# Performance work log

Measured on AMD Instinct MI355X. Metric: run time of the kernel, lower is better.

Reference implementation:

```python
import jax, jax.numpy as jnp
import numpy as np

COMMITMENT_COST = 0.25
NUM_EMBEDDINGS = 512
EMBEDDING_DIM = 64


def setup_inputs() -> dict:
    key = jax.random.key(0)
    k1, k2 = jax.random.split(key)
    inputs = jax.random.normal(k1, (32, EMBEDDING_DIM, 64, 64), dtype=jnp.float32)  # B,C,H,W
    embedding = jax.random.normal(k2, (NUM_EMBEDDINGS, EMBEDDING_DIM), dtype=jnp.float32)  # K,D
    return {"inputs": inputs, "embedding": embedding}


def reference(inputs, embedding):
    # Eval-mode forward of VectorQuantizerEMA (training-branch EMA updates are
    # in-place buffer updates, skipped when self.training is False).
    x = jnp.transpose(inputs, (0, 2, 3, 1))            # B,H,W,C
    B, H, W, D = x.shape
    K = embedding.shape[0]
    flat = x.reshape(-1, D)                            # N,D
    d = (jnp.sum(flat * flat, axis=1, keepdims=True)
         + jnp.sum(embedding * embedding, axis=1)
         - 2.0 * flat @ embedding.T)
    indices = jnp.argmin(d, axis=1)                    # N (int)
    # gather == one-hot @ embedding, but without materializing N x K one-hot
    quantized = embedding[indices].reshape(B, H, W, D)
    # commitment loss (quantized is detached in the torch code)
    e_latent_loss = jnp.mean((jax.lax.stop_gradient(quantized) - x) ** 2)
    loss = COMMITMENT_COST * e_latent_loss
    # straight-through estimator
    quantized_st = x + jax.lax.stop_gradient(quantized - x)
    # perplexity from encoding histogram (avg of one-hots = counts / N)
    counts = jnp.zeros((K,), dtype=flat.dtype).at[indices].add(1.0)
    avg_probs = counts / flat.shape[0]
    perplexity = jnp.exp(-jnp.sum(avg_probs * jnp.log(avg_probs + 1e-10)))
    out = jnp.transpose(quantized_st, (0, 3, 1, 2))    # B,C,H,W
    return loss, out, perplexity, indices
```

## Files before the change

kernel.cpp:

```cpp
#include <hip/hip_runtime.h>
#include <hip/hip_fp16.h>
#include <math.h>

#define NPIX   131072
#define KEMB   512
#define DDIM   64
#define HW     4096
#define BSTRIDE 262144

#define OUT_OFF  1
#define PERP_OFF 8388609
#define IDX_OFF  8388610

typedef __attribute__((ext_vector_type(8))) _Float16 f16x8;
typedef __attribute__((ext_vector_type(4))) float f32x4;


__global__ void vq_init(const float* __restrict__ emb, int* __restrict__ counts,
                        float* __restrict__ hnorms, float* __restrict__ loss_acc,
                        int* __restrict__ done_ctr,
                        unsigned short* __restrict__ eh_t,
                        unsigned short* __restrict__ el_t) {
    const int k = blockIdx.x;
    const int c = threadIdx.x;
    const int ct = k >> 4, cl = k & 15;
    const int ks = c >> 5, qd = (c >> 3) & 3, j = c & 7;
    float x = emb[k * DDIM + c];
    _Float16 h = (_Float16)x;
    float r1 = x - (float)h;
    _Float16 l = (_Float16)(r1 * 2048.0f);
    const int dst = ct * 1024 + ks * 512 + (qd * 16 + cl) * 8 + j;
    ((_Float16*)eh_t)[dst] = h;
    ((_Float16*)el_t)[dst] = l;
    float s = x * x;
#pragma unroll
    for (int off = 1; off <= 32; off <<= 1) s += __shfl_xor(s, off, 64);
    if (c == 0) {
        hnorms[k] = 0.5f * s;
        counts[k] = 0;
        if (k == 0) { *loss_acc = 0.f; *done_ctr = 0; }
    }
}

__global__ __launch_bounds__(1024, 4) void vq_main(
    const float* __restrict__ in, const float* __restrict__ emb,
    const unsigned short* __restrict__ eh_t, const unsigned short* __restrict__ el_t,
    const float* __restrict__ hnorms, int* __restrict__ counts,
    float* __restrict__ loss_acc, int* __restrict__ done_ctr,
    float* __restrict__ dout)
{
    __shared__ __align__(16) _Float16 eh_l[KEMB * DDIM];
    __shared__ __align__(16) _Float16 el_l[KEMB * DDIM];
    __shared__ __align__(16) float hn_lds[KEMB];
    __shared__ int hist[KEMB];
    __shared__ float part[8];
    __shared__ int lastflag;

    const int t    = threadIdx.x;
    const int lane = t & 63;
    const int wv   = t >> 6;
    const int quad = lane >> 4;
    const int col  = lane & 15;
    const int b    = blockIdx.x >> 3;
    const int p0   = ((blockIdx.x & 7) << 9) | (wv << 5);
    const float* xb = in + b * BSTRIDE;

    if (t < KEMB) hist[t] = 0;
    if (t < 128) ((float4*)hn_lds)[t] = ((const float4*)hnorms)[t];

#pragma unroll
    for (int i = 0; i < 4; ++i) {
        const int f = (t + i * 1024) * 8;
        *(f16x8*)&eh_l[f] = *(const f16x8*)((const _Float16*)eh_t + f);
        *(f16x8*)&el_l[f] = *(const f16x8*)((const _Float16*)el_t + f);
    }

    f16x8 xh[2][2], xl[2][2];
#pragma unroll
    for (int tt = 0; tt < 2; ++tt) {
#pragma unroll
        for (int s = 0; s < 2; ++s) {
            const int ppb = p0 + tt * 16 + col;
            const int c0  = s * 32 + quad * 8;
            f16x8 vh, vl;
#pragma unroll
            for (int j = 0; j < 8; ++j) {
                float x = xb[(c0 + j) * HW + ppb];
                _Float16 h = (_Float16)x;
                float r1 = x - (float)h;
                vh[j] = h;
                vl[j] = (_Float16)(r1 * 2048.0f);
            }
            xh[tt][s] = vh; xl[tt][s] = vl;
        }
    }

    __syncthreads();

    float v1[2], v2[2]; int k1[2], k2[2];
#pragma unroll
    for (int tt = 0; tt < 2; ++tt) {
        v1[tt] = 3.402823466e38f; v2[tt] = 3.402823466e38f; k1[tt] = 0; k2[tt] = 0;
    }

    for (int ct = 0; ct < 32; ++ct) {
        const int base = ct * 1024 + lane * 8;
        const f16x8 Ah0 = *(const f16x8*)&eh_l[base];
        const f16x8 Ah1 = *(const f16x8*)&eh_l[base + 512];
        const f16x8 Al0 = *(const f16x8*)&el_l[base];
        const f16x8 Al1 = *(const f16x8*)&el_l[base + 512];

        f32x4 a0h = (f32x4){0.f, 0.f, 0.f, 0.f};
        f32x4 a0l = (f32x4){0.f, 0.f, 0.f, 0.f};
        f32x4 a1h = (f32x4){0.f, 0.f, 0.f, 0.f};
        f32x4 a1l = (f32x4){0.f, 0.f, 0.f, 0.f};
        a0h = __builtin_amdgcn_mfma_f32_16x16x32_f16(Ah0, xh[0][0], a0h, 0, 0, 0);
        a0l = __builtin_amdgcn_mfma_f32_16x16x32_f16(Ah0, xl[0][0], a0l, 0, 0, 0);
        a0l = __builtin_amdgcn_mfma_f32_16x16x32_f16(Al0, xh[0][0], a0l, 0, 0, 0);
        a1h = __builtin_amdgcn_mfma_f32_16x16x32_f16(Ah0, xh[1][0], a1h, 0, 0, 0);
        a1l = __builtin_amdgcn_mfma_f32_16x16x32_f16(Ah0, xl[1][0], a1l, 0, 0, 0);
        a1l = __builtin_amdgcn_mfma_f32_16x16x32_f16(Al0, xh[1][0], a1l, 0, 0, 0);
        a0h = __builtin_amdgcn_mfma_f32_16x16x32_f16(Ah1, xh[0][1], a0h, 0, 0, 0);
        a0l = __builtin_amdgcn_mfma_f32_16x16x32_f16(Ah1, xl[0][1], a0l, 0, 0, 0);
        a0l = __builtin_amdgcn_mfma_f32_16x16x32_f16(Al1, xh[0][1], a0l, 0, 0, 0);
        a1h = __builtin_amdgcn_mfma_f32_16x16x32_f16(Ah1, xh[1][1], a1h, 0, 0, 0);
        a1l = __builtin_amdgcn_mfma_f32_16x16x32_f16(Ah1, xl[1][1], a1l, 0, 0, 0);
        a1l = __builtin_amdgcn_mfma_f32_16x16x32_f16(Al1, xh[1][1], a1l, 0, 0, 0);

        const f32x4 hn = *(const f32x4*)&hn_lds[ct * 16 + quad * 4];
#pragma unroll
        for (int r = 0; r < 4; ++r) {
            const int kk = ct * 16 + quad * 4 + r;
            float sc = hn[r] - (a0h[r] + a0l[r] * 4.8828125e-4f);
            if (sc < v1[0]) { v2[0] = v1[0]; k2[0] = k1[0]; v1[0] = sc; k1[0] = kk; }
            else if (sc < v2[0]) { v2[0] = sc; k2[0] = kk; }
            sc = hn[r] - (a1h[r] + a1l[r] * 4.8828125e-4f);
            if (sc < v1[1]) { v2[1] = v1[1]; k2[1] = k1[1]; v1[1] = sc; k1[1] = kk; }
            else if (sc < v2[1]) { v2[1] = sc; k2[1] = kk; }
        }
    }

#pragma unroll
    for (int tt = 0; tt < 2; ++tt) {
#pragma unroll
        for (int off = 16; off <= 32; off <<= 1) {
            float w1 = __shfl_xor(v1[tt], off, 64); int j1 = __shfl_xor(k1[tt], off, 64);
            float w2 = __shfl_xor(v2[tt], off, 64); int j2 = __shfl_xor(k2[tt], off, 64);
            bool aF = (v1[tt] < w1) || (v1[tt] == w1 && k1[tt] < j1);
            float t1 = aF ? v1[tt] : w1;  int u1 = aF ? k1[tt] : j1;
            float tl = aF ? w1 : v1[tt];  int ul = aF ? j1 : k1[tt];
            bool bS = (v2[tt] < w2) || (v2[tt] == w2 && k2[tt] < j2);
            float tc = bS ? v2[tt] : w2;  int uc = bS ? k2[tt] : j2;
            bool lS = (tl < tc) || (tl == tc && ul < uc);
            v1[tt] = t1; k1[tt] = u1;
            v2[tt] = lS ? tl : tc; k2[tt] = lS ? ul : uc;
        }
    }

    const int q    = lane & 31;
    const int pp   = p0 + q;
    const int tsel = (lane >> 4) & 1;
    const int kA = tsel ? k1[1] : k1[0];
    const int kB = tsel ? k2[1] : k2[0];

    const int kMine = (lane < 32) ? kA : kB;
    const float4* eM = (const float4*)(emb + kMine * DDIM);
    float a0 = hn_lds[kMine], a1 = 0.f, a2 = 0.f, a3 = 0.f;
#pragma unroll
    for (int i = 0; i < 16; ++i) {
        float4 ea = eM[i];
        const int c = i * 4;
        float x0 = xb[(c + 0) * HW + pp];
        float x1 = xb[(c + 1) * HW + pp];
        float x2 = xb[(c + 2) * HW + pp];
        float x3 = xb[(c + 3) * HW + pp];
        a0 = fmaf(-x0, ea.x, a0);
        a1 = fmaf(-x1, ea.y, a1);
        a2 = fmaf(-x2, ea.z, a2);
        a3 = fmaf(-x3, ea.w, a3);
    }
    const float dMine = (a0 + a1) + (a2 + a3);
    const float dOth  = __shfl_xor(dMine, 32, 64);
    const float dA = (lane < 32) ? dMine : dOth;
    const float dB = (lane < 32) ? dOth  : dMine;
    const int myk = (dB < dA || (dB == dA && kB < kA)) ? kB : kA;

    float lsum = 0.f;
    if (lane < 32) {
        dout[IDX_OFF + b * HW + pp] = (float)myk;
        atomicAdd(&hist[myk], 1);
        const float4* qrow = (const float4*)(emb + myk * DDIM);
        float* ob = dout + OUT_OFF + b * BSTRIDE;
#pragma unroll
        for (int i = 0; i < 16; ++i) {
            float4 qv = qrow[i];
            const int c = i * 4;
            float x0 = xb[(c + 0) * HW + pp];
            float x1 = xb[(c + 1) * HW + pp];
            float x2 = xb[(c + 2) * HW + pp];
            float x3 = xb[(c + 3) * HW + pp];
            float d0 = qv.x - x0;
            float d1 = qv.y - x1;
            float d2 = qv.z - x2;
            float d3 = qv.w - x3;
            lsum += d0 * d0 + d1 * d1 + d2 * d2 + d3 * d3;
            ob[(c + 0) * HW + pp] = x0 + d0;
            ob[(c + 1) * HW + pp] = x1 + d1;
            ob[(c + 2) * HW + pp] = x2 + d2;
            ob[(c + 3) * HW + pp] = x3 + d3;
        }
    }
    for (int off = 32; off > 0; off >>= 1) lsum += __shfl_down(lsum, off, 64);
    if (lane == 0) atomicAdd(loss_acc, lsum);

    __syncthreads();
    if (t < KEMB) {
        int v = hist[t];
        if (v) atomicAdd(&counts[t], v);
    }

    __syncthreads();
    if (t == 0) lastflag = (atomicAdd(done_ctr, 1) == 255) ? 1 : 0;
    __syncthreads();
    if (lastflag) {
        if (t < KEMB) {
            int cnt = atomicAdd(&counts[t], 0);
            float pa = (float)cnt / (float)NPIX;
            float v = pa * logf(pa + 1e-10f);
#pragma unroll
            for (int off = 1; off <= 32; off <<= 1) v += __shfl_xor(v, off, 64);
            if ((t & 63) == 0) part[t >> 6] = v;
        }
        __syncthreads();
        if (t == 0) {
            float s = 0.f;
#pragma unroll
            for (int i = 0; i < 8; ++i) s += part[i];
            dout[PERP_OFF] = expf(-s);
            dout[0] = 0.25f * atomicAdd(loss_acc, 0.0f) / 8388608.0f;
        }
    }
}

extern "C" void kernel_launch(void* const* d_in, const int* in_sizes, int n_in,
                              void* d_out, int out_size, void* d_ws, size_t ws_size,
                              hipStream_t stream) {
    const float* in  = (const float*)d_in[0];
    const float* emb = (const float*)d_in[1];
    float* dout = (float*)d_out;
    int*   counts   = (int*)d_ws;
    float* hnorms   = (float*)((char*)d_ws + 2048);
    float* loss_acc = (float*)((char*)d_ws + 4096);
    int*   done_ctr = (int*)((char*)d_ws + 4160);
    unsigned short* eh_t = (unsigned short*)((char*)d_ws + 8192);
    unsigned short* el_t = eh_t + KEMB * DDIM;

    vq_init<<<512, 64, 0, stream>>>(emb, counts, hnorms, loss_acc, done_ctr, eh_t, el_t);
    vq_main<<<256, 1024, 0, stream>>>(in, emb, eh_t, el_t, hnorms, counts, loss_acc, done_ctr, dout);
}
```

Baseline: 162.6 us.

## Software-pipeline codebook LDS loads and split top-2 select into two parity chains

Unrolls the distance loop by two codebook tiles and prefetches the next tile's fp16 fragments from LDS while the current tile's top-2 selection runs. Keeps separate top-2 state per parity so the two update chains are independent, and merges them before the cross-lane shuffle reduction. The branchy top-2 update becomes branchless code using fmed3/fminf and selects. The barrier now sits before the input conversion rather than after it, and the extra accumulators and state arrays raise register pressure under the 1024-thread launch bound.

```diff
diff --git a/kernel.cpp b/kernel.cpp
--- a/kernel.cpp
+++ b/kernel.cpp
@@ -42,6 +42,23 @@
     }
 }
 
+#define SELECT_UPDATE(PAR, TT, AH, AL, CT)                                   \
+    {                                                                        \
+        const f32x4 hn = *(const f32x4*)&hn_lds[(CT) * 16 + quad * 4];       \
+        _Pragma("unroll")                                                    \
+        for (int r = 0; r < 4; ++r) {                                        \
+            const int kk = (CT) * 16 + quad * 4 + r;                         \
+            const float sc = hn[r] - ((AH)[r] + (AL)[r] * 4.8828125e-4f);    \
+            const bool c1 = sc < v1[PAR][TT];                                \
+            const bool c2 = sc < v2[PAR][TT];                                \
+            const int nk2 = c1 ? k1[PAR][TT] : (c2 ? kk : k2[PAR][TT]);      \
+            const int nk1 = c1 ? kk : k1[PAR][TT];                           \
+            v2[PAR][TT] = __builtin_amdgcn_fmed3f(v1[PAR][TT], v2[PAR][TT], sc); \
+            v1[PAR][TT] = fminf(v1[PAR][TT], sc);                            \
+            k1[PAR][TT] = nk1; k2[PAR][TT] = nk2;                            \
+        }                                                                    \
+    }
+
 __global__ __launch_bounds__(1024, 4) void vq_main(
     const float* __restrict__ in, const float* __restrict__ emb,
     const unsigned short* __restrict__ eh_t, const unsigned short* __restrict__ el_t,
@@ -75,6 +92,8 @@
         *(f16x8*)&el_l[f] = *(const f16x8*)((const _Float16*)el_t + f);
     }
 
+    __syncthreads();
+
     f16x8 xh[2][2], xl[2][2];
 #pragma unroll
     for (int tt = 0; tt < 2; ++tt) {
@@ -95,21 +114,21 @@
         }
     }
 
-    __syncthreads();
-
-    float v1[2], v2[2]; int k1[2], k2[2];
-#pragma unroll
-    for (int tt = 0; tt < 2; ++tt) {
-        v1[tt] = 3.402823466e38f; v2[tt] = 3.402823466e38f; k1[tt] = 0; k2[tt] = 0;
-    }
-
-    for (int ct = 0; ct < 32; ++ct) {
-        const int base = ct * 1024 + lane * 8;
-        const f16x8 Ah0 = *(const f16x8*)&eh_l[base];
-        const f16x8 Ah1 = *(const f16x8*)&eh_l[base + 512];
-        const f16x8 Al0 = *(const f16x8*)&el_l[base];
-        const f16x8 Al1 = *(const f16x8*)&el_l[base + 512];
-
+    float v1[2][2], v2[2][2]; int k1[2][2], k2[2][2];
+#pragma unroll
+    for (int p = 0; p < 2; ++p)
+#pragma unroll
+        for (int tt = 0; tt < 2; ++tt) {
+            v1[p][tt] = 3.402823466e38f; v2[p][tt] = 3.402823466e38f;
+            k1[p][tt] = 0; k2[p][tt] = 0;
+        }
+
+    f16x8 Ah0 = *(const f16x8*)&eh_l[lane * 8];
+    f16x8 Ah1 = *(const f16x8*)&eh_l[lane * 8 + 512];
+    f16x8 Al0 = *(const f16x8*)&el_l[lane * 8];
+    f16x8 Al1 = *(const f16x8*)&el_l[lane * 8 + 512];
+
+    for (int ct = 0; ct < 32; ct += 2) {
         f32x4 a0h = (f32x4){0.f, 0.f, 0.f, 0.f};
         f32x4 a0l = (f32x4){0.f, 0.f, 0.f, 0.f};
         f32x4 a1h = (f32x4){0.f, 0.f, 0.f, 0.f};
@@ -127,41 +146,81 @@
         a1l = __builtin_amdgcn_mfma_f32_16x16x32_f16(Ah1, xl[1][1], a1l, 0, 0, 0);
         a1l = __builtin_amdgcn_mfma_f32_16x16x32_f16(Al1, xh[1][1], a1l, 0, 0, 0);
 
-        const f32x4 hn = *(const f32x4*)&hn_lds[ct * 16 + quad * 4];
-#pragma unroll
-        for (int r = 0; r < 4; ++r) {
-            const int kk = ct * 16 + quad * 4 + r;
-            float sc = hn[r] - (a0h[r] + a0l[r] * 4.8828125e-4f);
-            if (sc < v1[0]) { v2[0] = v1[0]; k2[0] = k1[0]; v1[0] = sc; k1[0] = kk; }
-            else if (sc < v2[0]) { v2[0] = sc; k2[0] = kk; }
-            sc = hn[r] - (a1h[r] + a1l[r] * 4.8828125e-4f);
-            if (sc < v1[1]) { v2[1] = v1[1]; k2[1] = k1[1]; v1[1] = sc; k1[1] = kk; }
-            else if (sc < v2[1]) { v2[1] = sc; k2[1] = kk; }
-        }
-    }
-
+        {
+            const int nbase = (ct + 1) * 1024 + lane * 8;
+            Ah0 = *(const f16x8*)&eh_l[nbase];
+            Ah1 = *(const f16x8*)&eh_l[nbase + 512];
+            Al0 = *(const f16x8*)&el_l[nbase];
+            Al1 = *(const f16x8*)&el_l[nbase + 512];
+        }
+
+        SELECT_UPDATE(0, 0, a0h, a0l, ct)
+        SELECT_UPDATE(0, 1, a1h, a1l, ct)
+
+        f32x4 b0h = (f32x4){0.f, 0.f, 0.f, 0.f};
+        f32x4 b0l = (f32x4){0.f, 0.f, 0.f, 0.f};
+        f32x4 b1h = (f32x4){0.f, 0.f, 0.f, 0.f};
+        f32x4 b1l = (f32x4){0.f, 0.f, 0.f, 0.f};
+        b0h = __builtin_amdgcn_mfma_f32_16x16x32_f16(Ah0, xh[0][0], b0h, 0, 0, 0);
+        b0l = __builtin_amdgcn_mfma_f32_16x16x32_f16(Ah0, xl[0][0], b0l, 0, 0, 0);
+        b0l = __builtin_amdgcn_mfma_f32_16x16x32_f16(Al0, xh[0][0], b0l, 0, 0, 0);
+        b1h = __builtin_amdgcn_mfma_f32_16x16x32_f16(Ah0, xh[1][0], b1h, 0, 0, 0);
+        b1l = __builtin_amdgcn_mfma_f32_16x16x32_f16(Ah0, xl[1][0], b1l, 0, 0, 0);
+        b1l = __builtin_amdgcn_mfma_f32_16x16x32_f16(Al0, xh[1][0], b1l, 0, 0, 0);
+        b0h = __builtin_amdgcn_mfma_f32_16x16x32_f16(Ah1, xh[0][1], b0h, 0, 0, 0);
+        b0l = __builtin_amdgcn_mfma_f32_16x16x32_f16(Ah1, xl[0][1], b0l, 0, 0, 0);
+        b0l = __builtin_amdgcn_mfma_f32_16x16x32_f16(Al1, xh[0][1], b0l, 0, 0, 0);
+        b1h = __builtin_amdgcn_mfma_f32_16x16x32_f16(Ah1, xh[1][1], b1h, 0, 0, 0);
+        b1l = __builtin_amdgcn_mfma_f32_16x16x32_f16(Ah1, xl[1][1], b1l, 0, 0, 0);
+        b1l = __builtin_amdgcn_mfma_f32_16x16x32_f16(Al1, xh[1][1], b1l, 0, 0, 0);
+
+        {
+            const int nbase = ((ct + 2) & 31) * 1024 + lane * 8;
+            Ah0 = *(const f16x8*)&eh_l[nbase];
+            Ah1 = *(const f16x8*)&eh_l[nbase + 512];
+            Al0 = *(const f16x8*)&el_l[nbase];
+            Al1 = *(const f16x8*)&el_l[nbase + 512];
+        }
+
+        SELECT_UPDATE(1, 0, b0h, b0l, ct + 1)
+        SELECT_UPDATE(1, 1, b1h, b1l, ct + 1)
+    }
+
+    float V1[2], V2[2]; int K1[2], K2[2];
 #pragma unroll
     for (int tt = 0; tt < 2; ++tt) {
+        bool aF = (v1[0][tt] < v1[1][tt]) || (v1[0][tt] == v1[1][tt] && k1[0][tt] < k1[1][tt]);
+        float t1 = aF ? v1[0][tt] : v1[1][tt];  int u1 = aF ? k1[0][tt] : k1[1][tt];
+        float tl = aF ? v1[1][tt] : v1[0][tt];  int ul = aF ? k1[1][tt] : k1[0][tt];
+        bool bS = (v2[0][tt] < v2[1][tt]) || (v2[0][tt] == v2[1][tt] && k2[0][tt] < k2[1][tt]);
+        float tc = bS ? v2[0][tt] : v2[1][tt];  int uc = bS ? k2[0][tt] : k2[1][tt];
+        bool lS = (tl < tc) || (tl == tc && ul < uc);
+        V1[tt] = t1; K1[tt] = u1;
+        V2[tt] = lS ? tl : tc; K2[tt] = lS ? ul : uc;
+    }
+
+#pragma unroll
+    for (int tt = 0; tt < 2; ++tt) {
 #pragma unroll
         for (int off = 16; off <= 32; off <<= 1) {
-            float w1 = __shfl_xor(v1[tt], off, 64); int j1 = __shfl_xor(k1[tt], off, 64);
-            float w2 = __shfl_xor(v2[tt], off, 64); int j2 = __shfl_xor(k2[tt], off, 64);
-            bool aF = (v1[tt] < w1) || (v1[tt] == w1 && k1[tt] < j1);
-            float t1 = aF ? v1[tt] : w1;  int u1 = aF ? k1[tt] : j1;
-            float tl = aF ? w1 : v1[tt];  int ul = aF ? j1 : k1[tt];
-            bool bS = (v2[tt] < w2) || (v2[tt] == w2 && k2[tt] < j2);
-            float tc = bS ? v2[tt] : w2;  int uc = bS ? k2[tt] : j2;
+            float w1 = __shfl_xor(V1[tt], off, 64); int j1 = __shfl_xor(K1[tt], off, 64);
+            float w2 = __shfl_xor(V2[tt], off, 64); int j2 = __shfl_xor(K2[tt], off, 64);
+            bool aF = (V1[tt] < w1) || (V1[tt] == w1 && K1[tt] < j1);
+            float t1 = aF ? V1[tt] : w1;  int u1 = aF ? K1[tt] : j1;
+            float tl = aF ? w1 : V1[tt];  int ul = aF ? j1 : K1[tt];
+            bool bS = (V2[tt] < w2) || (V2[tt] == w2 && K2[tt] < j2);
+            float tc = bS ? V2[tt] : w2;  int uc = bS ? K2[tt] : j2;
             bool lS = (tl < tc) || (tl == tc && ul < uc);
-            v1[tt] = t1; k1[tt] = u1;
-            v2[tt] = lS ? tl : tc; k2[tt] = lS ? ul : uc;
+            V1[tt] = t1; K1[tt] = u1;
+            V2[tt] = lS ? tl : tc; K2[tt] = lS ? ul : uc;
         }
     }
 
     const int q    = lane & 31;
     const int pp   = p0 + q;
     const int tsel = (lane >> 4) & 1;
-    const int kA = tsel ? k1[1] : k1[0];
-    const int kB = tsel ? k2[1] : k2[0];
+    const int kA = tsel ? K1[1] : K1[0];
+    const int kB = tsel ? K2[1] : K2[0];
 
     const int kMine = (lane < 32) ? kA : kB;
     const float4* eM = (const float4*)(emb + kMine * DDIM);
```

Result: faster. 154.2 us (-5.1%).
